# Performance work log

Measured on AMD Instinct MI355X. Metric: run time of the kernel, lower is better.

## Reference

```python
import jax, jax.numpy as jnp
import numpy as np

B = 32; SEQ = 900; GRID = 30; PFX = 16; D = 512
H = 8; HD = 64; WS = 3; SS = 1
NW = (GRID // WS) ** 2; N = WS * WS
INTER = 1536  # find_multiple(round(4.0*512*2/3), 256)
EPS = 1e-5
SCALE = HD ** -0.5


def _rel_pos_index():
    coords = np.stack(np.meshgrid(np.arange(WS), np.arange(WS), indexing='ij')).reshape(2, -1)
    rel = (coords[:, :, None] - coords[:, None, :]).transpose(1, 2, 0).copy()
    rel[:, :, 0] += WS - 1
    rel[:, :, 1] += WS - 1
    rel[:, :, 0] *= 2 * WS - 1
    return rel.sum(-1)  # [N, N]


def _attn_mask():
    img = np.zeros((GRID, GRID))
    cnt = 0
    sl = (slice(0, -WS), slice(-WS, -SS), slice(-SS, None))
    for h in sl:
        for w in sl:
            img[h, w] = cnt
            cnt += 1
    mw = img.reshape(GRID // WS, WS, GRID // WS, WS).transpose(0, 2, 1, 3).reshape(-1, N)
    diff = mw[:, None, :] - mw[:, :, None]
    return np.where(diff != 0, -100.0, 0.0).astype(np.float32)  # [nW, N, N]


REL_IDX = _rel_pos_index()
MASK = _attn_mask()


def rms_norm(x):
    xf = x.astype(jnp.float32)
    v = jnp.mean(xf * xf, -1, keepdims=True)
    return (xf * jax.lax.rsqrt(v + EPS)).astype(x.dtype)


def swiglu(x, gu_w, down_w):
    gu = x @ gu_w.T
    gate, up = gu[..., :INTER], gu[..., INTER:]
    return (jax.nn.silu(gate) * up) @ down_w.T


def setup_inputs() -> dict:
    key = jax.random.key(0)
    ks = jax.random.split(key, 8)
    s = 0.02
    return {
        'hidden_states': jax.random.normal(ks[0], (B, PFX + SEQ, D), jnp.float32),
        'qkv_w': jax.random.normal(ks[1], (3 * D, D), jnp.float32) * s,
        'qkv_b': jnp.zeros((3 * D,), jnp.float32),
        'proj_w': jax.random.normal(ks[2], (D, D), jnp.float32) * s,
        'proj_b': jnp.zeros((D,), jnp.float32),
        'rel_bias': jax.random.normal(ks[3], ((2 * WS - 1) ** 2, H), jnp.float32) * s,
        'gu_w': jax.random.normal(ks[4], (2 * INTER, D), jnp.float32) * s,
        'down_w': jax.random.normal(ks[5], (D, INTER), jnp.float32) * s,
        'pgu_w': jax.random.normal(ks[6], (2 * INTER, D), jnp.float32) * s,
        'pdown_w': jax.random.normal(ks[7], (D, INTER), jnp.float32) * s,
    }


def reference(hidden_states, qkv_w, qkv_b, proj_w, proj_b, rel_bias, gu_w, down_w, pgu_w, pdown_w):
    hs = hidden_states
    prefix = hs[:, :PFX]                                     # [B, 16, D]
    grid = hs[:, PFX:] + jnp.mean(prefix, 1, keepdims=True)  # broadcast prefix mean
    x = grid.reshape(B, GRID, GRID, D)
    residual = x
    # cyclic shift
    x = jnp.roll(x, (-SS, -SS), (1, 2))
    # window partition -> [B*nW, N, D]
    xw = x.reshape(B, GRID // WS, WS, GRID // WS, WS, D).transpose(0, 1, 3, 2, 4, 5).reshape(B * NW, N, D)
    qkv = (xw @ qkv_w.T + qkv_b).reshape(B * NW, N, 3, H, HD).transpose(2, 0, 3, 1, 4)
    q, k, v = qkv[0] * SCALE, qkv[1], qkv[2]                 # [B*nW, H, N, HD]
    attn = jnp.einsum('whid,whjd->whij', q, k)
    bias = rel_bias[jnp.asarray(REL_IDX).reshape(-1)].reshape(N, N, H).transpose(2, 0, 1)
    attn = attn + bias[None]
    attn = attn.reshape(B, NW, H, N, N) + jnp.asarray(MASK)[None, :, None]
    attn = jax.nn.softmax(attn.reshape(B * NW, H, N, N), -1)
    out = jnp.einsum('whij,whjd->whid', attn, v).transpose(0, 2, 1, 3).reshape(B * NW, N, D)
    out = out @ proj_w.T + proj_b
    # window reverse + reverse shift
    x = out.reshape(B, GRID // WS, GRID // WS, WS, WS, D).transpose(0, 1, 3, 2, 4, 5).reshape(B, GRID, GRID, D)
    x = jnp.roll(x, (SS, SS), (1, 2))
    x = rms_norm(residual.reshape(B, SEQ, D) + x.reshape(B, SEQ, D))
    prefix = rms_norm(prefix + swiglu(prefix, pgu_w, pdown_w))
    hs = jnp.concatenate([prefix, x], 1)
    return rms_norm(hs + swiglu(hs, gu_w, down_w))
```

## Files before the change

### kernel.cpp

```cpp
#include <hip/hip_runtime.h>
#include <cstdint>
#include <cstddef>

typedef float f32x4 __attribute__((ext_vector_type(4)));
typedef short s16x8 __attribute__((ext_vector_type(8)));
typedef short s16x4 __attribute__((ext_vector_type(4)));

#define DEV static __device__ __forceinline__

DEV float bf2f(short s) {
  union { unsigned u; float f; } c;
  c.u = ((unsigned)(unsigned short)s) << 16;
  return c.f;
}
DEV short f2bf(float f) {
  union { float f; unsigned u; } c;
  c.f = f;
  unsigned r = c.u + 0x7fffu + ((c.u >> 16) & 1u);
  return (short)(r >> 16);
}
DEV float wave_allsum(float v) {
#pragma unroll
  for (int off = 32; off > 0; off >>= 1) v += __shfl_xor(v, off, 64);
  return v;
}
DEV void gload_lds16(const void* g, void* l) {
  __builtin_amdgcn_global_load_lds(
      (const __attribute__((address_space(1))) void*)g,
      (__attribute__((address_space(3))) void*)l, 16, 0, 0);
}
DEV float silu_f(float g) { return g / (1.f + __expf(-g)); }

DEV int xcd_swizzle(int orig, int nwg) {
  int q = nwg >> 3, r = nwg & 7;
  int xcd = orig & 7, pos = orig >> 3;
  return (xcd < r ? xcd * (q + 1) : r * (q + 1) + (xcd - r) * q) + pos;
}

DEV void sync_phase() {
  asm volatile("s_waitcnt vmcnt(0)" ::: "memory");
  __builtin_amdgcn_s_barrier();
  __builtin_amdgcn_sched_barrier(0);
}

enum { EPI_BF16 = 0, EPI_BIAS_BF16 = 1, EPI_SCATTER = 4, EPI_ADDOUT = 5, EPI_GU = 6 };

template <int EPI>
__global__ __launch_bounds__(256) void gemm2(
    const short* __restrict__ A, const short* __restrict__ W,
    const short* __restrict__ Wu, const float* __restrict__ bias,
    void* __restrict__ outp, int M, int N, int K)
{
  __shared__ short As0[8192], Bs0[8192];
  __shared__ short As1[8192], Bs1[8192];
  const int tid = threadIdx.x;
  const int wave = tid >> 6, lane = tid & 63;
  const int nwg = gridDim.x * gridDim.y;
  const int orig = blockIdx.y * gridDim.x + blockIdx.x;
  const int wg = xcd_swizzle(orig, nwg);
  const int bx = wg % gridDim.x, by = wg / gridDim.x;
  const int row0 = by * 128;
  const int col0 = (EPI == EPI_GU) ? bx * 64 : bx * 128;
  const int wr = wave >> 1, wc = wave & 1;

  f32x4 acc[4][4];
#pragma unroll
  for (int m = 0; m < 4; ++m)
#pragma unroll
    for (int n = 0; n < 4; ++n) acc[m][n] = f32x4{0.f, 0.f, 0.f, 0.f};

  const short* aptr[4];
  const short* bptr[4];
  int ldst[4];
#pragma unroll
  for (int i = 0; i < 4; ++i) {
    int e = i * 2048 + tid * 8;
    int srow = e >> 6;
    int skg = ((e >> 3) & 7) ^ (srow & 7);
    aptr[i] = A + (size_t)(row0 + srow) * K + skg * 8;
    if (EPI == EPI_GU)
      bptr[i] = (srow < 64 ? W + (size_t)(col0 + srow) * K
                           : Wu + (size_t)(col0 + srow - 64) * K) + skg * 8;
    else
      bptr[i] = W + (size_t)(col0 + srow) * K + skg * 8;
    ldst[i] = i * 2048 + wave * 512;
  }

#define STAGE(AS, BS, KT)                                   \
  do {                                                      \
    _Pragma("unroll") for (int i = 0; i < 4; ++i)           \
        gload_lds16(aptr[i] + (KT), &AS[ldst[i]]);          \
    _Pragma("unroll") for (int i = 0; i < 4; ++i)           \
        gload_lds16(bptr[i] + (KT), &BS[ldst[i]]);          \
  } while (0)

#define COMPUTE(AS, BS)                                                        \
  do {                                                                         \
    _Pragma("unroll") for (int ks = 0; ks < 2; ++ks) {                         \
      s16x8 af[4], bfr[4];                                                     \
      _Pragma("unroll") for (int m = 0; m < 4; ++m) {                          \
        int row = wr * 64 + m * 16 + (lane & 15);                              \
        int kg = (ks * 4 + (lane >> 4)) ^ (row & 7);                           \
        af[m] = *(const s16x8*)&AS[row * 64 + kg * 8];                         \
      }                                                                        \
      _Pragma("unroll") for (int n = 0; n < 4; ++n) {                          \
        int brow = (EPI == EPI_GU)                                             \
                       ? ((n < 2 ? wc * 32 + n * 16                            \
                                 : 64 + wc * 32 + (n - 2) * 16) + (lane & 15)) \
                       : (wc * 64 + n * 16 + (lane & 15));                     \
        int kg = (ks * 4 + (lane >> 4)) ^ (brow & 7);                          \
        bfr[n] = *(const s16x8*)&BS[brow * 64 + kg * 8];                       \
      }                                                                        \
      _Pragma("unroll") for (int m = 0; m < 4; ++m)                            \
          _Pragma("unroll") for (int n = 0; n < 4; ++n)                        \
              acc[m][n] = __builtin_amdgcn_mfma_f32_16x16x32_bf16(             \
                  af[m], bfr[n], acc[m][n], 0, 0, 0);                          \
    }                                                                          \
  } while (0)

  STAGE(As0, Bs0, 0);
  sync_phase();
  for (int kt = 0; kt < K; kt += 128) {
    STAGE(As1, Bs1, kt + 64);
    COMPUTE(As0, Bs0);
    sync_phase();
    if (kt + 128 < K) STAGE(As0, Bs0, kt + 128);
    COMPUTE(As1, Bs1);
    if (kt + 128 < K) sync_phase();
  }
#undef STAGE
#undef COMPUTE

  const int lr = (lane >> 4) * 4, lc = lane & 15;
#pragma unroll
  for (int m = 0; m < 4; ++m) {
#pragma unroll
    for (int i = 0; i < 4; ++i) {
      int gr = row0 + wr * 64 + m * 16 + lr + i;
      size_t orow;
      if (EPI == EPI_SCATTER) {
        int b = gr / 900, rem = gr % 900;
        int w = rem / 9, n_ = rem % 9;
        int wi = w / 10, wj = w % 10;
        int ii = n_ / 3, jj = n_ % 3;
        int gy = wi * 3 + ii + 1; if (gy >= 30) gy -= 30;
        int gx = wj * 3 + jj + 1; if (gx >= 30) gx -= 30;
        orow = (size_t)b * 900 + gy * 30 + gx;
      } else {
        orow = (size_t)gr;
      }
      if (EPI == EPI_GU) {
#pragma unroll
        for (int n = 0; n < 2; ++n) {
          int gc = col0 + wc * 32 + n * 16 + lc;
          float v = silu_f(acc[m][n][i]) * acc[m][n + 2][i];
          ((short*)outp)[orow * (size_t)N + gc] = f2bf(v);
        }
      } else {
#pragma unroll
        for (int n = 0; n < 4; ++n) {
          int gc = col0 + wc * 64 + n * 16 + lc;
          float v = acc[m][n][i];
          if (EPI == EPI_BIAS_BF16 || EPI == EPI_SCATTER) v += bias[gc];
          if (EPI == EPI_ADDOUT) {
            float* po = (float*)outp;
            size_t oi = orow * (size_t)N + gc;
            po[oi] = po[oi] + v;
          } else {
            ((short*)outp)[orow * (size_t)N + gc] = f2bf(v);
          }
        }
      }
    }
  }
}

__global__ __launch_bounds__(256) void cvt4_kernel(const float* __restrict__ src,
                                                   short* __restrict__ dst, int n4) {
  int i = blockIdx.x * 256 + threadIdx.x;
  if (i >= n4) return;
  f32x4 v = *(const f32x4*)(src + (size_t)i * 4);
  s16x4 o;
#pragma unroll
  for (int e = 0; e < 4; ++e) o[e] = f2bf(v[e]);
  *(s16x4*)(dst + (size_t)i * 4) = o;
}

__global__ __launch_bounds__(256) void prefix_cvt_kernel(const float* __restrict__ hs,
                                                         short* __restrict__ dst) {
  int i = blockIdx.x * 256 + threadIdx.x;
  if (i >= 512 * 128) return;
  int r = i >> 7, c4 = i & 127;
  int b = r >> 4, t = r & 15;
  f32x4 v = *(const f32x4*)(hs + ((size_t)b * 916 + t) * 512 + c4 * 4);
  s16x4 o;
#pragma unroll
  for (int e = 0; e < 4; ++e) o[e] = f2bf(v[e]);
  *(s16x4*)(dst + (size_t)r * 512 + c4 * 4) = o;
}

__global__ __launch_bounds__(512) void mean_kernel(const float* __restrict__ hs,
                                                   float* __restrict__ m) {
  int b = blockIdx.x, d = threadIdx.x;
  float s = 0.f;
#pragma unroll
  for (int t = 0; t < 16; ++t) s += hs[((size_t)b * 916 + t) * 512 + d];
  m[b * 512 + d] = s * (1.f / 16.f);
}

__global__ __launch_bounds__(256) void prep_kernel(const float* __restrict__ hs,
                                                   const float* __restrict__ m,
                                                   float* __restrict__ gridf,
                                                   short* __restrict__ xw) {
  int idx = blockIdx.x * 256 + threadIdx.x;
  if (idx >= 32 * 900 * 128) return;
  int c4 = idx & 127;
  int row = idx >> 7;
  int b = row / 900, rem = row % 900;
  int gy = rem / 30, gx = rem % 30;
  f32x4 v = *(const f32x4*)(hs + ((size_t)b * 916 + 16 + rem) * 512 + c4 * 4);
  f32x4 mm = *(const f32x4*)(m + b * 512 + c4 * 4);
  v += mm;
  *(f32x4*)(gridf + (size_t)row * 512 + c4 * 4) = v;
  int ry = gy + 29; if (ry >= 30) ry -= 30;
  int rx = gx + 29; if (rx >= 30) rx -= 30;
  int wi = ry / 3, ii = ry % 3, wj = rx / 3, jj = rx % 3;
  size_t xrow = (size_t)((b * 100 + wi * 10 + wj) * 9 + ii * 3 + jj);
  s16x4 o;
#pragma unroll
  for (int e = 0; e < 4; ++e) o[e] = f2bf(v[e]);
  *(s16x4*)(xw + xrow * 512 + c4 * 4) = o;
}

__global__ __launch_bounds__(256) void attn_kernel(const short* __restrict__ qkv,
                                                   const float* __restrict__ rel_bias,
                                                   short* __restrict__ outp) {
  __shared__ short sq[9 * 512];
  __shared__ short sk[9 * 512];
  __shared__ short sv[9 * 512];
  __shared__ float sS[648];
  const int wlin = blockIdx.x;
  const int w = wlin % 100;
  const int wi = w / 10, wj = w % 10;
  const int tid = threadIdx.x;
  const short* base = qkv + (size_t)wlin * 9 * 1536;
  for (int idx = tid; idx < 1728; idx += 256) {
    int n = idx / 192, c8 = idx % 192;
    s16x8 v = *(const s16x8*)(base + (size_t)n * 1536 + c8 * 8);
    int which = c8 >> 6;
    short* dst = (which == 0) ? sq : (which == 1) ? sk : sv;
    *(s16x8*)(dst + n * 512 + (c8 & 63) * 8) = v;
  }
  __syncthreads();
  for (int idx = tid; idx < 648; idx += 256) {
    int h = idx / 81, r = idx % 81, i = r / 9, j = r % 9;
    const short* qp = sq + i * 512 + h * 64;
    const short* kp = sk + j * 512 + h * 64;
    float dot = 0.f;
#pragma unroll
    for (int c = 0; c < 8; ++c) {
      s16x8 qv = *(const s16x8*)(qp + c * 8);
      s16x8 kv = *(const s16x8*)(kp + c * 8);
#pragma unroll
      for (int e = 0; e < 8; ++e) dot += bf2f(qv[e]) * bf2f(kv[e]);
    }
    float s = dot * 0.125f;
    int ia = i / 3, ja = i % 3, ib = j / 3, jb = j % 3;
    s += rel_bias[(5 * (ia - ib + 2) + (ja - jb + 2)) * 8 + h];
    int ra = wi * 3 + ia, ca = wj * 3 + ja, rb = wi * 3 + ib, cb = wj * 3 + jb;
    int rga = (ra < 27) ? 0 : (ra < 29) ? 1 : 2;
    int cga = (ca < 27) ? 0 : (ca < 29) ? 1 : 2;
    int rgb = (rb < 27) ? 0 : (rb < 29) ? 1 : 2;
    int cgb = (cb < 27) ? 0 : (cb < 29) ? 1 : 2;
    if (rga * 3 + cga != rgb * 3 + cgb) s -= 100.f;
    sS[idx] = s;
  }
  __syncthreads();
  if (tid < 72) {
    float* row = sS + tid * 9;
    float mx = row[0];
#pragma unroll
    for (int j = 1; j < 9; ++j) mx = fmaxf(mx, row[j]);
    float e[9], sum = 0.f;
#pragma unroll
    for (int j = 0; j < 9; ++j) { e[j] = __expf(row[j] - mx); sum += e[j]; }
    float inv = 1.f / sum;
#pragma unroll
    for (int j = 0; j < 9; ++j) row[j] = e[j] * inv;
  }
  __syncthreads();
  for (int idx = tid; idx < 576; idx += 256) {
    int h = idx / 72, r = idx % 72, i = r / 8, d8 = r % 8;
    const float* p = sS + (h * 9 + i) * 9;
    float a[8] = {0, 0, 0, 0, 0, 0, 0, 0};
#pragma unroll
    for (int j = 0; j < 9; ++j) {
      float pj = p[j];
      s16x8 vv = *(const s16x8*)(sv + j * 512 + h * 64 + d8 * 8);
#pragma unroll
      for (int e = 0; e < 8; ++e) a[e] += pj * bf2f(vv[e]);
    }
    s16x8 o;
#pragma unroll
    for (int e = 0; e < 8; ++e) o[e] = f2bf(a[e]);
    *(s16x8*)(outp + ((size_t)wlin * 9 + i) * 512 + h * 64 + d8 * 8) = o;
  }
}

__global__ __launch_bounds__(64) void addnorm1_kernel(const float* __restrict__ g,
                                                      const short* __restrict__ p,
                                                      float* __restrict__ out,
                                                      short* __restrict__ hsb) {
  int row = blockIdx.x, lane = threadIdx.x;
  size_t off = (size_t)row * 512;
  f32x4 x[2];
  float ss = 0.f;
#pragma unroll
  for (int i = 0; i < 2; ++i) {
    f32x4 a = *(const f32x4*)(g + off + i * 256 + lane * 4);
    s16x4 b = *(const s16x4*)(p + off + i * 256 + lane * 4);
#pragma unroll
    for (int e = 0; e < 4; ++e) a[e] += bf2f(b[e]);
    x[i] = a;
    ss += a[0] * a[0] + a[1] * a[1] + a[2] * a[2] + a[3] * a[3];
  }
  ss = wave_allsum(ss);
  float sc = rsqrtf(ss * (1.f / 512.f) + 1e-5f);
  int b_ = row / 900, t = row % 900;
  size_t orow = ((size_t)b_ * 916 + 16 + t) * 512;
#pragma unroll
  for (int i = 0; i < 2; ++i) {
    f32x4 y = x[i] * sc;
    *(f32x4*)(out + orow + i * 256 + lane * 4) = y;
    s16x4 o;
#pragma unroll
    for (int e = 0; e < 4; ++e) o[e] = f2bf(y[e]);
    *(s16x4*)(hsb + orow + i * 256 + lane * 4) = o;
  }
}

__global__ __launch_bounds__(64) void prefix_addnorm_kernel(const float* __restrict__ hs,
                                                            const short* __restrict__ pd,
                                                            float* __restrict__ out,
                                                            short* __restrict__ hsb) {
  int r = blockIdx.x, lane = threadIdx.x;
  int b = r >> 4, t = r & 15;
  size_t orow = ((size_t)b * 916 + t) * 512;
  f32x4 x[2];
  float ss = 0.f;
#pragma unroll
  for (int i = 0; i < 2; ++i) {
    f32x4 a = *(const f32x4*)(hs + orow + i * 256 + lane * 4);
    s16x4 d = *(const s16x4*)(pd + (size_t)r * 512 + i * 256 + lane * 4);
#pragma unroll
    for (int e = 0; e < 4; ++e) a[e] += bf2f(d[e]);
    x[i] = a;
    ss += a[0] * a[0] + a[1] * a[1] + a[2] * a[2] + a[3] * a[3];
  }
  ss = wave_allsum(ss);
  float sc = rsqrtf(ss * (1.f / 512.f) + 1e-5f);
#pragma unroll
  for (int i = 0; i < 2; ++i) {
    f32x4 y = x[i] * sc;
    *(f32x4*)(out + orow + i * 256 + lane * 4) = y;
    s16x4 o;
#pragma unroll
    for (int e = 0; e < 4; ++e) o[e] = f2bf(y[e]);
    *(s16x4*)(hsb + orow + i * 256 + lane * 4) = o;
  }
}

__global__ __launch_bounds__(64) void final_addnorm_kernel(float* __restrict__ io) {
  int row = blockIdx.x, lane = threadIdx.x;
  size_t off = (size_t)row * 512;
  f32x4 x[2];
  float ss = 0.f;
#pragma unroll
  for (int i = 0; i < 2; ++i) {
    f32x4 a = *(const f32x4*)(io + off + i * 256 + lane * 4);
    x[i] = a;
    ss += a[0] * a[0] + a[1] * a[1] + a[2] * a[2] + a[3] * a[3];
  }
  ss = wave_allsum(ss);
  float sc = rsqrtf(ss * (1.f / 512.f) + 1e-5f);
#pragma unroll
  for (int i = 0; i < 2; ++i)
    *(f32x4*)(io + off + i * 256 + lane * 4) = x[i] * sc;
}

static constexpr size_t OFF_WQKV   = 0;
static constexpr size_t OFF_WPROJ  = 1572864;
static constexpr size_t OFF_WGU    = 2097152;
static constexpr size_t OFF_WDOWN  = 5242880;
static constexpr size_t OFF_WPGU   = 6815744;
static constexpr size_t OFF_WPDOWN = 9961472;
static constexpr size_t OFF_MEAN   = 11534336;
static constexpr size_t OFF_PREFB  = 11599872;
static constexpr size_t OFF_PINTER = 13697024;
static constexpr size_t OFF_PDOUT  = 15269888;
static constexpr size_t OFF_GRIDF  = 16777216;
static constexpr size_t OFF_XW     = 75759616;
static constexpr size_t OFF_QKV    = 105250816;
static constexpr size_t OFF_ATTNO  = OFF_XW;
static constexpr size_t OFF_PROJS  = OFF_QKV;
static constexpr size_t OFF_INTER  = OFF_GRIDF;
static constexpr size_t OFF_HSB    = 193724416;

extern "C" void kernel_launch(void* const* d_in, const int* in_sizes, int n_in,
                              void* d_out, int out_size, void* d_ws, size_t ws_size,
                              hipStream_t stream) {
  const float* hs      = (const float*)d_in[0];
  const float* qkv_w   = (const float*)d_in[1];
  const float* qkv_b   = (const float*)d_in[2];
  const float* proj_w  = (const float*)d_in[3];
  const float* proj_b  = (const float*)d_in[4];
  const float* rel_b   = (const float*)d_in[5];
  const float* gu_w    = (const float*)d_in[6];
  const float* down_w  = (const float*)d_in[7];
  const float* pgu_w   = (const float*)d_in[8];
  const float* pdown_w = (const float*)d_in[9];

  char* ws = (char*)d_ws;
  short* Wqkv   = (short*)(ws + OFF_WQKV);
  short* Wproj  = (short*)(ws + OFF_WPROJ);
  short* Wgu    = (short*)(ws + OFF_WGU);
  short* Wdown  = (short*)(ws + OFF_WDOWN);
  short* Wpgu   = (short*)(ws + OFF_WPGU);
  short* Wpdown = (short*)(ws + OFF_WPDOWN);
  float* meanb  = (float*)(ws + OFF_MEAN);
  short* prefb  = (short*)(ws + OFF_PREFB);
  short* pinter = (short*)(ws + OFF_PINTER);
  short* pdout  = (short*)(ws + OFF_PDOUT);
  float* gridf  = (float*)(ws + OFF_GRIDF);
  short* xw     = (short*)(ws + OFF_XW);
  short* qkvb   = (short*)(ws + OFF_QKV);
  short* attno  = (short*)(ws + OFF_ATTNO);
  short* projs  = (short*)(ws + OFF_PROJS);
  short* interb = (short*)(ws + OFF_INTER);
  short* hsb    = (short*)(ws + OFF_HSB);
  float* outf   = (float*)d_out;

  cvt4_kernel<<<768, 256, 0, stream>>>(qkv_w, Wqkv, 786432 / 4);
  cvt4_kernel<<<256, 256, 0, stream>>>(proj_w, Wproj, 262144 / 4);
  cvt4_kernel<<<1536, 256, 0, stream>>>(gu_w, Wgu, 1572864 / 4);
  cvt4_kernel<<<768, 256, 0, stream>>>(down_w, Wdown, 786432 / 4);
  cvt4_kernel<<<1536, 256, 0, stream>>>(pgu_w, Wpgu, 1572864 / 4);
  cvt4_kernel<<<768, 256, 0, stream>>>(pdown_w, Wpdown, 786432 / 4);
  prefix_cvt_kernel<<<256, 256, 0, stream>>>(hs, prefb);

  mean_kernel<<<32, 512, 0, stream>>>(hs, meanb);
  prep_kernel<<<14400, 256, 0, stream>>>(hs, meanb, gridf, xw);

  gemm2<EPI_BIAS_BF16><<<dim3(12, 225), 256, 0, stream>>>(
      xw, Wqkv, nullptr, qkv_b, qkvb, 28800, 1536, 512);
  attn_kernel<<<3200, 256, 0, stream>>>(qkvb, rel_b, attno);

  gemm2<EPI_SCATTER><<<dim3(4, 225), 256, 0, stream>>>(
      attno, Wproj, nullptr, proj_b, projs, 28800, 512, 512);
  addnorm1_kernel<<<28800, 64, 0, stream>>>(gridf, projs, outf, hsb);

  gemm2<EPI_GU><<<dim3(24, 4), 256, 0, stream>>>(
      prefb, Wpgu, Wpgu + 1536 * 512, nullptr, pinter, 512, 1536, 512);
  gemm2<EPI_BF16><<<dim3(4, 4), 256, 0, stream>>>(
      pinter, Wpdown, nullptr, nullptr, pdout, 512, 512, 1536);
  prefix_addnorm_kernel<<<512, 64, 0, stream>>>(hs, pdout, outf, hsb);

  gemm2<EPI_GU><<<dim3(24, 229), 256, 0, stream>>>(
      hsb, Wgu, Wgu + 1536 * 512, nullptr, interb, 29312, 1536, 512);
  gemm2<EPI_ADDOUT><<<dim3(4, 229), 256, 0, stream>>>(
      interb, Wdown, nullptr, nullptr, outf, 29312, 512, 1536);
  final_addnorm_kernel<<<29312, 64, 0, stream>>>(outf);

  (void)in_sizes; (void)n_in; (void)out_size; (void)ws_size;
}
```

Baseline: 495.3 us.

## Add 256x256 eight-wave GEMM kernel with interleaved loads; store residual grid as bf16

Adds a new 512-thread GEMM (gemm8) with 256x256 output tiles, swizzled LDS, finely interleaved global-to-LDS loads with partial waitcnt gates, and MFMA priority boosting. The four large GEMMs (QKV, proj scatter, gate-up, down) now use it, which raises arithmetic intensity and cuts barrier overhead per MFMA. The GU epilogue exchanges gate/up accumulators through LDS. Separately, the residual grid is stored as bf16 instead of fp32, halving that buffer's traffic at some precision cost in the residual add. Out-of-range rows at the M tail are guarded, since 113/115 row tiles overshoot M.

Measured after the change: 490.1 us. About the same (-1.0%).

```diff
diff --git a/kernel.cpp b/kernel.cpp
--- a/kernel.cpp
+++ b/kernel.cpp
@@ -44,6 +44,194 @@
 }
 
 enum { EPI_BF16 = 0, EPI_BIAS_BF16 = 1, EPI_SCATTER = 4, EPI_ADDOUT = 5, EPI_GU = 6 };
+
+template <int EPI>
+__global__ __launch_bounds__(512, 2) void gemm8(
+    const short* __restrict__ A, const short* __restrict__ W,
+    const short* __restrict__ Wu, const float* __restrict__ bias,
+    void* __restrict__ outp, int M, int N, int K)
+{
+  __shared__ short lds[65536];
+  const int tid = threadIdx.x;
+  const int wid = tid >> 6, lane = tid & 63;
+  const int wr = wid >> 2, wc = wid & 3;
+  const int nwg = gridDim.x * gridDim.y;
+  const int orig = blockIdx.y * gridDim.x + blockIdx.x;
+  const int wg = xcd_swizzle(orig, nwg);
+  const int bx = wg % gridDim.x, by = wg / gridDim.x;
+  const int row0 = by * 256;
+
+  f32x4 acc[8][4];
+#pragma unroll
+  for (int m = 0; m < 8; ++m)
+#pragma unroll
+    for (int n = 0; n < 4; ++n) acc[m][n] = f32x4{0.f, 0.f, 0.f, 0.f};
+
+  const int srow = tid >> 3;
+  const int k8s = (tid & 7) ^ (srow & 7);
+  const short* aub[4];
+  const short* bub[4];
+#pragma unroll
+  for (int u = 0; u < 4; ++u)
+    aub[u] = A + (size_t)(row0 + u * 64 + srow) * K + k8s * 8;
+  if (EPI == EPI_GU) {
+    const int colg = bx * 128;
+#pragma unroll
+    for (int u = 0; u < 2; ++u) {
+      bub[u]     = W  + (size_t)(colg + u * 64 + srow) * K + k8s * 8;
+      bub[u + 2] = Wu + (size_t)(colg + u * 64 + srow) * K + k8s * 8;
+    }
+  } else {
+    const int c0 = bx * 256;
+#pragma unroll
+    for (int u = 0; u < 4; ++u)
+      bub[u] = W + (size_t)(c0 + u * 64 + srow) * K + k8s * 8;
+  }
+  const int ldw = wid * 512;
+
+#define SA(d, u, kt) gload_lds16(aub[u] + (kt), &lds[(d)*16384 + (u)*4096 + ldw])
+#define SB(d, u, kt) gload_lds16(bub[u] + (kt), &lds[32768 + (d)*16384 + (u)*4096 + ldw])
+#define GATE(VN)                                              \
+  asm volatile("s_waitcnt vmcnt(" #VN ")" ::: "memory");      \
+  __builtin_amdgcn_s_barrier();
+
+  const int kg0 = (lane >> 4) ^ (lane & 7);
+  const int kg1 = (4 + (lane >> 4)) ^ (lane & 7);
+  const int aoff = (wr * 128 + (lane & 15)) * 64;
+  const int boff = 32768 + (wc * 64 + (lane & 15)) * 64;
+
+#define READ_B(d)                                                              \
+  _Pragma("unroll") for (int n = 0; n < 4; ++n) {                              \
+    bfr[0][n] = *(const s16x8*)&lds[(d)*16384 + boff + n * 1024 + kg0 * 8];    \
+    bfr[1][n] = *(const s16x8*)&lds[(d)*16384 + boff + n * 1024 + kg1 * 8];    \
+  }
+#define DO_PHASE(d, p)                                                         \
+  do {                                                                         \
+    s16x8 a00 = *(const s16x8*)&lds[(d)*16384 + aoff + (2*(p))*1024 + kg0*8];  \
+    s16x8 a01 = *(const s16x8*)&lds[(d)*16384 + aoff + (2*(p))*1024 + kg1*8];  \
+    s16x8 a10 = *(const s16x8*)&lds[(d)*16384 + aoff + (2*(p)+1)*1024 + kg0*8];\
+    s16x8 a11 = *(const s16x8*)&lds[(d)*16384 + aoff + (2*(p)+1)*1024 + kg1*8];\
+    __builtin_amdgcn_s_setprio(1);                                             \
+    _Pragma("unroll") for (int n = 0; n < 4; ++n)                              \
+      acc[2*(p)][n] = __builtin_amdgcn_mfma_f32_16x16x32_bf16(a00, bfr[0][n], acc[2*(p)][n], 0, 0, 0); \
+    _Pragma("unroll") for (int n = 0; n < 4; ++n)                              \
+      acc[2*(p)+1][n] = __builtin_amdgcn_mfma_f32_16x16x32_bf16(a10, bfr[0][n], acc[2*(p)+1][n], 0, 0, 0); \
+    _Pragma("unroll") for (int n = 0; n < 4; ++n)                              \
+      acc[2*(p)][n] = __builtin_amdgcn_mfma_f32_16x16x32_bf16(a01, bfr[1][n], acc[2*(p)][n], 0, 0, 0); \
+    _Pragma("unroll") for (int n = 0; n < 4; ++n)                              \
+      acc[2*(p)+1][n] = __builtin_amdgcn_mfma_f32_16x16x32_bf16(a11, bfr[1][n], acc[2*(p)+1][n], 0, 0, 0); \
+    __builtin_amdgcn_s_setprio(0);                                             \
+  } while (0)
+
+  SB(0, 0, 0); SB(0, 1, 0); SB(0, 2, 0); SB(0, 3, 0);
+  SA(0, 0, 0); SA(0, 2, 0); SA(0, 1, 0); SA(0, 3, 0);
+
+  const int NT = K >> 6;
+  for (int t = 0; t < NT - 1; ++t) {
+    const int d = t & 1, d1 = d ^ 1;
+    const int kn = (t + 1) * 64;
+    s16x8 bfr[2][4];
+    SB(d1, 0, kn); SB(d1, 1, kn);
+    GATE(4);
+    READ_B(d);
+    DO_PHASE(d, 0);
+    SB(d1, 2, kn); SB(d1, 3, kn);
+    DO_PHASE(d, 1);
+    SA(d1, 0, kn); SA(d1, 2, kn);
+    GATE(6);
+    DO_PHASE(d, 2);
+    SA(d1, 1, kn); SA(d1, 3, kn);
+    DO_PHASE(d, 3);
+  }
+  {
+    const int d = (NT - 1) & 1;
+    s16x8 bfr[2][4];
+    GATE(2);
+    READ_B(d);
+    DO_PHASE(d, 0);
+    DO_PHASE(d, 1);
+    GATE(0);
+    DO_PHASE(d, 2);
+    DO_PHASE(d, 3);
+  }
+#undef SA
+#undef SB
+#undef GATE
+#undef READ_B
+#undef DO_PHASE
+
+  const int li = lane >> 4, lc = lane & 15;
+  if (EPI == EPI_GU) {
+    float* fbuf = (float*)lds;
+    __syncthreads();
+    if (wc >= 2) {
+      const int off = (wr * 2 + (wc - 2)) * 8192;
+#pragma unroll
+      for (int m = 0; m < 8; ++m)
+#pragma unroll
+        for (int i = 0; i < 4; ++i)
+#pragma unroll
+          for (int n = 0; n < 4; ++n)
+            fbuf[off + (m * 16 + li * 4 + i) * 64 + n * 16 + lc] = acc[m][n][i];
+    }
+    __syncthreads();
+    if (wc < 2) {
+      const int off = (wr * 2 + wc) * 8192;
+      const int colg = bx * 128;
+#pragma unroll
+      for (int m = 0; m < 8; ++m) {
+#pragma unroll
+        for (int i = 0; i < 4; ++i) {
+          int gr = row0 + wr * 128 + m * 16 + li * 4 + i;
+          if (gr < M) {
+#pragma unroll
+            for (int n = 0; n < 4; ++n) {
+              float u = fbuf[off + (m * 16 + li * 4 + i) * 64 + n * 16 + lc];
+              float g = acc[m][n][i];
+              ((short*)outp)[(size_t)gr * N + colg + wc * 64 + n * 16 + lc] =
+                  f2bf(silu_f(g) * u);
+            }
+          }
+        }
+      }
+    }
+  } else {
+    const int c0 = bx * 256;
+#pragma unroll
+    for (int m = 0; m < 8; ++m) {
+#pragma unroll
+      for (int i = 0; i < 4; ++i) {
+        int gr = row0 + wr * 128 + m * 16 + li * 4 + i;
+        if (gr >= M) continue;
+        size_t orow;
+        if (EPI == EPI_SCATTER) {
+          int b = gr / 900, rem = gr % 900;
+          int w = rem / 9, n_ = rem % 9;
+          int wi = w / 10, wj = w % 10;
+          int ii = n_ / 3, jj = n_ % 3;
+          int gy = wi * 3 + ii + 1; if (gy >= 30) gy -= 30;
+          int gx = wj * 3 + jj + 1; if (gx >= 30) gx -= 30;
+          orow = (size_t)b * 900 + gy * 30 + gx;
+        } else {
+          orow = (size_t)gr;
+        }
+#pragma unroll
+        for (int n = 0; n < 4; ++n) {
+          int gc = c0 + wc * 64 + n * 16 + lc;
+          float v = acc[m][n][i];
+          if (EPI == EPI_BIAS_BF16 || EPI == EPI_SCATTER) v += bias[gc];
+          if (EPI == EPI_ADDOUT) {
+            float* po = (float*)outp;
+            size_t oi = orow * (size_t)N + gc;
+            po[oi] = po[oi] + v;
+          } else {
+            ((short*)outp)[orow * (size_t)N + gc] = f2bf(v);
+          }
+        }
+      }
+    }
+  }
+}
 
 template <int EPI>
 __global__ __launch_bounds__(256) void gemm2(
@@ -137,38 +325,19 @@
 #pragma unroll
     for (int i = 0; i < 4; ++i) {
       int gr = row0 + wr * 64 + m * 16 + lr + i;
-      size_t orow;
-      if (EPI == EPI_SCATTER) {
-        int b = gr / 900, rem = gr % 900;
-        int w = rem / 9, n_ = rem % 9;
-        int wi = w / 10, wj = w % 10;
-        int ii = n_ / 3, jj = n_ % 3;
-        int gy = wi * 3 + ii + 1; if (gy >= 30) gy -= 30;
-        int gx = wj * 3 + jj + 1; if (gx >= 30) gx -= 30;
-        orow = (size_t)b * 900 + gy * 30 + gx;
-      } else {
-        orow = (size_t)gr;
-      }
       if (EPI == EPI_GU) {
 #pragma unroll
         for (int n = 0; n < 2; ++n) {
           int gc = col0 + wc * 32 + n * 16 + lc;
           float v = silu_f(acc[m][n][i]) * acc[m][n + 2][i];
-          ((short*)outp)[orow * (size_t)N + gc] = f2bf(v);
+          ((short*)outp)[(size_t)gr * N + gc] = f2bf(v);
         }
       } else {
 #pragma unroll
         for (int n = 0; n < 4; ++n) {
           int gc = col0 + wc * 64 + n * 16 + lc;
           float v = acc[m][n][i];
-          if (EPI == EPI_BIAS_BF16 || EPI == EPI_SCATTER) v += bias[gc];
-          if (EPI == EPI_ADDOUT) {
-            float* po = (float*)outp;
-            size_t oi = orow * (size_t)N + gc;
-            po[oi] = po[oi] + v;
-          } else {
-            ((short*)outp)[orow * (size_t)N + gc] = f2bf(v);
-          }
+          ((short*)outp)[(size_t)gr * N + gc] = f2bf(v);
         }
       }
     }
@@ -210,7 +379,7 @@
 
 __global__ __launch_bounds__(256) void prep_kernel(const float* __restrict__ hs,
                                                    const float* __restrict__ m,
-                                                   float* __restrict__ gridf,
+                                                   short* __restrict__ gridb,
                                                    short* __restrict__ xw) {
   int idx = blockIdx.x * 256 + threadIdx.x;
   if (idx >= 32 * 900 * 128) return;
@@ -221,14 +390,14 @@
   f32x4 v = *(const f32x4*)(hs + ((size_t)b * 916 + 16 + rem) * 512 + c4 * 4);
   f32x4 mm = *(const f32x4*)(m + b * 512 + c4 * 4);
   v += mm;
-  *(f32x4*)(gridf + (size_t)row * 512 + c4 * 4) = v;
+  s16x4 o;
+#pragma unroll
+  for (int e = 0; e < 4; ++e) o[e] = f2bf(v[e]);
+  *(s16x4*)(gridb + (size_t)row * 512 + c4 * 4) = o;
   int ry = gy + 29; if (ry >= 30) ry -= 30;
   int rx = gx + 29; if (rx >= 30) rx -= 30;
   int wi = ry / 3, ii = ry % 3, wj = rx / 3, jj = rx % 3;
   size_t xrow = (size_t)((b * 100 + wi * 10 + wj) * 9 + ii * 3 + jj);
-  s16x4 o;
-#pragma unroll
-  for (int e = 0; e < 4; ++e) o[e] = f2bf(v[e]);
   *(s16x4*)(xw + xrow * 512 + c4 * 4) = o;
 }
 
@@ -307,36 +476,34 @@
   }
 }
 
-__global__ __launch_bounds__(64) void addnorm1_kernel(const float* __restrict__ g,
+__global__ __launch_bounds__(64) void addnorm1_kernel(const short* __restrict__ g,
                                                       const short* __restrict__ p,
                                                       float* __restrict__ out,
                                                       short* __restrict__ hsb) {
   int row = blockIdx.x, lane = threadIdx.x;
-  size_t off = (size_t)row * 512;
-  f32x4 x[2];
+  size_t off = (size_t)row * 512 + lane * 8;
+  s16x8 a8 = *(const s16x8*)(g + off);
+  s16x8 b8 = *(const s16x8*)(p + off);
+  float x[8];
   float ss = 0.f;
 #pragma unroll
-  for (int i = 0; i < 2; ++i) {
-    f32x4 a = *(const f32x4*)(g + off + i * 256 + lane * 4);
-    s16x4 b = *(const s16x4*)(p + off + i * 256 + lane * 4);
-#pragma unroll
-    for (int e = 0; e < 4; ++e) a[e] += bf2f(b[e]);
-    x[i] = a;
-    ss += a[0] * a[0] + a[1] * a[1] + a[2] * a[2] + a[3] * a[3];
+  for (int e = 0; e < 8; ++e) {
+    x[e] = bf2f(a8[e]) + bf2f(b8[e]);
+    ss += x[e] * x[e];
   }
   ss = wave_allsum(ss);
   float sc = rsqrtf(ss * (1.f / 512.f) + 1e-5f);
   int b_ = row / 900, t = row % 900;
-  size_t orow = ((size_t)b_ * 916 + 16 + t) * 512;
-#pragma unroll
-  for (int i = 0; i < 2; ++i) {
-    f32x4 y = x[i] * sc;
-    *(f32x4*)(out + orow + i * 256 + lane * 4) = y;
-    s16x4 o;
-#pragma unroll
-    for (int e = 0; e < 4; ++e) o[e] = f2bf(y[e]);
-    *(s16x4*)(hsb + orow + i * 256 + lane * 4) = o;
-  }
+  size_t orow = ((size_t)b_ * 916 + 16 + t) * 512 + lane * 8;
+  s16x8 o;
+#pragma unroll
+  for (int e = 0; e < 8; ++e) {
+    x[e] *= sc;
+    o[e] = f2bf(x[e]);
+  }
+  *(f32x4*)(out + orow) = f32x4{x[0], x[1], x[2], x[3]};
+  *(f32x4*)(out + orow + 4) = f32x4{x[4], x[5], x[6], x[7]};
+  *(s16x8*)(hsb + orow) = o;
 }
 
 __global__ __launch_bounds__(64) void prefix_addnorm_kernel(const float* __restrict__ hs,
@@ -398,13 +565,13 @@
 static constexpr size_t OFF_PREFB  = 11599872;
 static constexpr size_t OFF_PINTER = 13697024;
 static constexpr size_t OFF_PDOUT  = 15269888;
-static constexpr size_t OFF_GRIDF  = 16777216;
-static constexpr size_t OFF_XW     = 75759616;
-static constexpr size_t OFF_QKV    = 105250816;
+static constexpr size_t OFF_GRIDB  = 16777216;
+static constexpr size_t OFF_XW     = 46268416;
+static constexpr size_t OFF_QKV    = 75890688;
 static constexpr size_t OFF_ATTNO  = OFF_XW;
 static constexpr size_t OFF_PROJS  = OFF_QKV;
-static constexpr size_t OFF_INTER  = OFF_GRIDF;
-static constexpr size_t OFF_HSB    = 193724416;
+static constexpr size_t OFF_INTER  = OFF_GRIDB;
+static constexpr size_t OFF_HSB    = 164364288;
 
 extern "C" void kernel_launch(void* const* d_in, const int* in_sizes, int n_in,
                               void* d_out, int out_size, void* d_ws, size_t ws_size,
@@ -431,7 +598,7 @@
   short* prefb  = (short*)(ws + OFF_PREFB);
   short* pinter = (short*)(ws + OFF_PINTER);
   short* pdout  = (short*)(ws + OFF_PDOUT);
-  float* gridf  = (float*)(ws + OFF_GRIDF);
+  short* gridb  = (short*)(ws + OFF_GRIDB);
   short* xw     = (short*)(ws + OFF_XW);
   short* qkvb   = (short*)(ws + OFF_QKV);
   short* attno  = (short*)(ws + OFF_ATTNO);
@@ -449,15 +616,15 @@
   prefix_cvt_kernel<<<256, 256, 0, stream>>>(hs, prefb);
 
   mean_kernel<<<32, 512, 0, stream>>>(hs, meanb);
-  prep_kernel<<<14400, 256, 0, stream>>>(hs, meanb, gridf, xw);
-
-  gemm2<EPI_BIAS_BF16><<<dim3(12, 225), 256, 0, stream>>>(
+  prep_kernel<<<14400, 256, 0, stream>>>(hs, meanb, gridb, xw);
+
+  gemm8<EPI_BIAS_BF16><<<dim3(6, 113), 512, 0, stream>>>(
       xw, Wqkv, nullptr, qkv_b, qkvb, 28800, 1536, 512);
   attn_kernel<<<3200, 256, 0, stream>>>(qkvb, rel_b, attno);
 
-  gemm2<EPI_SCATTER><<<dim3(4, 225), 256, 0, stream>>>(
+  gemm8<EPI_SCATTER><<<dim3(2, 113), 512, 0, stream>>>(
       attno, Wproj, nullptr, proj_b, projs, 28800, 512, 512);
-  addnorm1_kernel<<<28800, 64, 0, stream>>>(gridf, projs, outf, hsb);
+  addnorm1_kernel<<<28800, 64, 0, stream>>>(gridb, projs, outf, hsb);
 
   gemm2<EPI_GU><<<dim3(24, 4), 256, 0, stream>>>(
       prefb, Wpgu, Wpgu + 1536 * 512, nullptr, pinter, 512, 1536, 512);
@@ -465,9 +632,9 @@
       pinter, Wpdown, nullptr, nullptr, pdout, 512, 512, 1536);
   prefix_addnorm_kernel<<<512, 64, 0, stream>>>(hs, pdout, outf, hsb);
 
-  gemm2<EPI_GU><<<dim3(24, 229), 256, 0, stream>>>(
+  gemm8<EPI_GU><<<dim3(12, 115), 512, 0, stream>>>(
       hsb, Wgu, Wgu + 1536 * 512, nullptr, interb, 29312, 1536, 512);
-  gemm2<EPI_ADDOUT><<<dim3(4, 229), 256, 0, stream>>>(
+  gemm8<EPI_ADDOUT><<<dim3(2, 115), 512, 0, stream>>>(
       interb, Wdown, nullptr, nullptr, outf, 29312, 512, 1536);
   final_addnorm_kernel<<<29312, 64, 0, stream>>>(outf);
 
```
